# Kernel optimization log

Measured on AMD Instinct MI355X. Metric: run time of the kernel, lower is better.

The kernel has to match this reference:

```python
import jax, jax.numpy as jnp
import numpy as np

B, S, H, N, D = 2, 2048, 1024, 16, 64  # batch, seq, hidden, heads, head_dim


def setup_inputs() -> dict:
    key = jax.random.key(0)
    ks = jax.random.split(key, 7)
    sc = 0.02
    return {
        "query": jax.random.normal(ks[0], (B, S, H), jnp.float32),
        "key": jax.random.normal(ks[1], (B, S, H), jnp.float32),
        "value": jax.random.normal(ks[2], (B, S, H), jnp.float32),
        "Wq": jax.random.normal(ks[3], (N, H, D), jnp.float32) * sc,
        "Wk": jax.random.normal(ks[4], (N, H, D), jnp.float32) * sc,
        "Wv": jax.random.normal(ks[5], (N, H, D), jnp.float32) * sc,
        "Wo": jax.random.normal(ks[6], (H, H), jnp.float32) * sc,
    }


def reference(query, key, value, Wq, Wk, Wv, Wo):
    # Per-head projections (all heads batched): q,k,v -> [B, N, S, D]
    q = jnp.einsum('bsh,nhd->bnsd', query, Wq)
    k = jnp.einsum('bsh,nhd->bnsd', key, Wk)
    v = jnp.einsum('bsh,nhd->bnsd', value, Wv)
    scale = jnp.sqrt(jnp.asarray(D, q.dtype))
    # scaled dot-product attention, no mask, dropout=0 (eval mode)
    scores = jnp.einsum('bnqd,bnkd->bnqk', q, k) / scale  # [B, N, S, S]
    attn = jax.nn.softmax(scores, axis=-1)
    ctx = jnp.einsum('bnqk,bnkd->bnqd', attn, v)  # [B, N, S, D]
    # concat heads (head order matches the module's per-head list order)
    concat = ctx.transpose(0, 2, 1, 3).reshape(B, S, N * D)  # [B, S, H]
    out = concat @ Wo  # output projection, bias-free
    return out, attn
```

## Files before the change

kernel.cpp:

```cpp
#include <hip/hip_runtime.h>
#include <hip/hip_bf16.h>

using bf16 = __hip_bfloat16;
typedef __bf16 bf16x8 __attribute__((ext_vector_type(8)));
typedef __bf16 bf16x4 __attribute__((ext_vector_type(4)));
typedef float f32x4 __attribute__((ext_vector_type(4)));

__device__ __forceinline__ void async16(const void* g, void* l) {
    __builtin_amdgcn_global_load_lds((const __attribute__((address_space(1))) void*)g,
                                     (__attribute__((address_space(3))) void*)l, 16, 0, 0);
}
__device__ __forceinline__ bf16x8 ld8(const bf16* p) {
    return *reinterpret_cast<const bf16x8*>(p);
}
__device__ __forceinline__ unsigned short bfbits(float f) {
    bf16 h = __float2bfloat16(f);
    return *reinterpret_cast<unsigned short*>(&h);
}


__global__ __launch_bounds__(256) void cast_kernel(const float* __restrict__ q, const float* __restrict__ k,
                                                   const float* __restrict__ v, bf16* __restrict__ dst) {
    int z = blockIdx.z;
    const float* src = (z == 0) ? q : (z == 1) ? k : v;
    bf16* d = dst + (size_t)z * 4194304u;
    size_t i = ((size_t)blockIdx.x * 256 + threadIdx.x) * 4;
    float4 f = *(const float4*)(src + i);
    ushort4 pk = make_ushort4(bfbits(f.x), bfbits(f.y), bfbits(f.z), bfbits(f.w));
    *(ushort4*)(d + i) = pk;
}

__global__ __launch_bounds__(256) void wt_kernel(const float* __restrict__ wq, const float* __restrict__ wk,
                                                 const float* __restrict__ wv, bf16* __restrict__ wt) {
    int z = blockIdx.z;
    const float* W = (z == 0) ? wq : (z == 1) ? wk : wv;
    bf16* Wt = wt + (size_t)z * (1024u * 1024u);
    int n = blockIdx.y, h0 = blockIdx.x * 64;
    __shared__ float tile[64][65];
    int t = threadIdx.x, row = t >> 2, cq = t & 3;
#pragma unroll
    for (int u = 0; u < 4; u++) {
        int col = cq * 16 + u * 4;
        float4 f = *(const float4*)(W + (size_t)(n * 1024 + h0 + row) * 64 + col);
        tile[row][col] = f.x; tile[row][col + 1] = f.y; tile[row][col + 2] = f.z; tile[row][col + 3] = f.w;
    }
    __syncthreads();
#pragma unroll
    for (int u = 0; u < 4; u++) {
        int hl = cq * 16 + u * 4;
        ushort4 pk = make_ushort4(bfbits(tile[hl][row]), bfbits(tile[hl + 1][row]),
                                  bfbits(tile[hl + 2][row]), bfbits(tile[hl + 3][row]));
        *(ushort4*)(Wt + (size_t)(n * 64 + row) * 1024 + h0 + hl) = pk;
    }
}

__global__ __launch_bounds__(256) void wo_kernel(const float* __restrict__ Wo, bf16* __restrict__ Wot) {
    int h0 = blockIdx.x * 64, j0 = blockIdx.y * 64;
    __shared__ float tile[64][65];
    int t = threadIdx.x, row = t >> 2, cq = t & 3;
#pragma unroll
    for (int u = 0; u < 4; u++) {
        int col = cq * 16 + u * 4;
        float4 f = *(const float4*)(Wo + (size_t)(h0 + row) * 1024 + j0 + col);
        tile[row][col] = f.x; tile[row][col + 1] = f.y; tile[row][col + 2] = f.z; tile[row][col + 3] = f.w;
    }
    __syncthreads();
#pragma unroll
    for (int u = 0; u < 4; u++) {
        int hl = cq * 16 + u * 4;
        ushort4 pk = make_ushort4(bfbits(tile[hl][row]), bfbits(tile[hl + 1][row]),
                                  bfbits(tile[hl + 2][row]), bfbits(tile[hl + 3][row]));
        *(ushort4*)(Wot + (size_t)(j0 + row) * 1024 + h0 + hl) = pk;
    }
}

__global__ __launch_bounds__(256) void proj_kernel(const bf16* __restrict__ Xall, const bf16* __restrict__ Wall,
                                                   bf16* __restrict__ qb, bf16* __restrict__ kb,
                                                   bf16* __restrict__ vt) {
    int z = blockIdx.z;
    const bf16* X = Xall + (size_t)z * (4096u * 1024u);
    const bf16* W = Wall + (size_t)z * (1024u * 1024u);
    __shared__ bf16 sA[128 * 64];
    __shared__ bf16 sB[128 * 64];
    int t = threadIdx.x, lane = t & 63, q4 = lane >> 4, cl = lane & 15, w = t >> 6;
    int wm = (w >> 1) * 64, wn = (w & 1) * 64;
    int m0 = blockIdx.x * 128, n0 = blockIdx.y * 128;
    f32x4 acc[4][4] = {};
    for (int k0 = 0; k0 < 1024; k0 += 64) {
#pragma unroll
        for (int it = 0; it < 4; it++) {
            int j = it * 256 + t;
            int row = j >> 3, sl = j & 7, g = sl ^ (row & 7);
            async16(X + (size_t)(m0 + row) * 1024 + k0 + g * 8, sA + j * 8);
            async16(W + (size_t)(n0 + row) * 1024 + k0 + g * 8, sB + j * 8);
        }
        __syncthreads();
#pragma unroll
        for (int ks = 0; ks < 2; ks++) {
            bf16x8 af[4], bfr[4];
#pragma unroll
            for (int mi = 0; mi < 4; mi++) {
                int row = wm + mi * 16 + cl;
                af[mi] = ld8(sA + row * 64 + ((ks * 4 + q4) ^ (row & 7)) * 8);
            }
#pragma unroll
            for (int ni = 0; ni < 4; ni++) {
                int row = wn + ni * 16 + cl;
                bfr[ni] = ld8(sB + row * 64 + ((ks * 4 + q4) ^ (row & 7)) * 8);
            }
#pragma unroll
            for (int mi = 0; mi < 4; mi++)
#pragma unroll
                for (int ni = 0; ni < 4; ni++)
                    acc[mi][ni] = __builtin_amdgcn_mfma_f32_16x16x32_bf16(af[mi], bfr[ni], acc[mi][ni], 0, 0, 0);
        }
        __syncthreads();
    }
    if (z < 2) {
        bf16* dst = (z == 0) ? qb : kb;
        float qs = (z == 0) ? 0.18033688011112042f : 1.0f;
#pragma unroll
        for (int mi = 0; mi < 4; mi++)
#pragma unroll
            for (int ni = 0; ni < 4; ni++) {
                int col = n0 + wn + ni * 16 + cl;
                int hn = col >> 6, dd = col & 63;
#pragma unroll
                for (int i = 0; i < 4; i++) {
                    int row = m0 + wm + mi * 16 + q4 * 4 + i;
                    int b = row >> 11, s = row & 2047;
                    dst[(size_t)((b * 16 + hn) * 2048 + s) * 64 + dd] = __float2bfloat16(acc[mi][ni][i] * qs);
                }
            }
    } else {
#pragma unroll
        for (int mi = 0; mi < 4; mi++)
#pragma unroll
            for (int ni = 0; ni < 4; ni++) {
                int col = n0 + wn + ni * 16 + cl;
                int hn = col >> 6, dd = col & 63;
                int row0 = m0 + wm + mi * 16 + q4 * 4;
                int b = row0 >> 11, s = row0 & 2047;
                ushort4 pk = make_ushort4(bfbits(acc[mi][ni][0]), bfbits(acc[mi][ni][1]),
                                          bfbits(acc[mi][ni][2]), bfbits(acc[mi][ni][3]));
                *(ushort4*)(vt + (size_t)((b * 16 + hn) * 64 + dd) * 2048 + s) = pk;
            }
    }
}

__global__ __launch_bounds__(256) void attn_kernel(const bf16* __restrict__ qb, const bf16* __restrict__ kb,
                                                   const bf16* __restrict__ vt, bf16* __restrict__ cc,
                                                   float* __restrict__ attn) {
    __shared__ bf16 sQP[64 * 64];
    __shared__ bf16 sKb[64 * 64];
    __shared__ bf16 sVb[2][64 * 64];
    __shared__ float srow[64];
    __shared__ float sinv[64];
    int t = threadIdx.x, lane = t & 63, q4 = lane >> 4, cl = lane & 15, w = t >> 6;
    int bn = blockIdx.x;
    int s0 = blockIdx.y * 64;
    const bf16* qh = qb + (size_t)bn * 2048 * 64;
    const bf16* kh = kb + (size_t)bn * 2048 * 64;
    const bf16* vh = vt + (size_t)bn * 64 * 2048;
    float* ah = attn + (size_t)bn * 2048 * 2048;

    if (t < 64) srow[t] = 0.f;
#pragma unroll
    for (int it = 0; it < 2; it++) {
        int j = it * 256 + t;
        int row = j >> 3, sl = j & 7, g = sl ^ (row & 7);
        async16(qh + (size_t)(s0 + row) * 64 + g * 8, sQP + j * 8);
        async16(kh + (size_t)row * 64 + g * 8, sKb + j * 8);
    }
    __syncthreads();

    bf16x8 aq[4][2];
#pragma unroll
    for (int mi = 0; mi < 4; mi++)
#pragma unroll
        for (int ks = 0; ks < 2; ks++) {
            int row = mi * 16 + cl;
            aq[mi][ks] = ld8(sQP + row * 64 + ((ks * 4 + q4) ^ (row & 7)) * 8);
        }

    float rs[4][4] = {};
    for (int ch = 0; ch < 32; ch++) {
        const bf16* kcur = (ch & 1) ? sVb[0] : sKb;
        bf16* knxt = (ch & 1) ? sKb : sVb[0];
        if (ch < 31) {
#pragma unroll
            for (int it = 0; it < 2; it++) {
                int j = it * 256 + t;
                int row = j >> 3, sl = j & 7, g = sl ^ (row & 7);
                async16(kh + (size_t)((ch + 1) * 64 + row) * 64 + g * 8, knxt + j * 8);
            }
        }
        bf16x8 bk[2];
#pragma unroll
        for (int ks = 0; ks < 2; ks++) {
            int row = w * 16 + cl;
            bk[ks] = ld8(kcur + row * 64 + ((ks * 4 + q4) ^ (row & 7)) * 8);
        }
#pragma unroll
        for (int mi = 0; mi < 4; mi++) {
            f32x4 sa = {0.f, 0.f, 0.f, 0.f};
            sa = __builtin_amdgcn_mfma_f32_16x16x32_bf16(aq[mi][0], bk[0], sa, 0, 0, 0);
            sa = __builtin_amdgcn_mfma_f32_16x16x32_bf16(aq[mi][1], bk[1], sa, 0, 0, 0);
#pragma unroll
            for (int i = 0; i < 4; i++) rs[mi][i] += exp2f(sa[i]);
        }
        __syncthreads();
    }
#pragma unroll
    for (int mi = 0; mi < 4; mi++)
#pragma unroll
        for (int i = 0; i < 4; i++) {
            float v = rs[mi][i];
            v += __shfl_xor(v, 1);
            v += __shfl_xor(v, 2);
            v += __shfl_xor(v, 4);
            v += __shfl_xor(v, 8);
            if (cl == 0) atomicAdd(&srow[mi * 16 + q4 * 4 + i], v);
        }
    __syncthreads();
    if (t < 64) sinv[t] = 1.0f / srow[t];
    __syncthreads();
    float invC[4];
#pragma unroll
    for (int i = 0; i < 4; i++) invC[i] = sinv[w * 16 + q4 * 4 + i];

#pragma unroll
    for (int it = 0; it < 2; it++) {
        int j = it * 256 + t;
        int row = j >> 3, sl = j & 7, g = sl ^ (row & 7);
        async16(kh + (size_t)row * 64 + g * 8, sKb + j * 8);
        async16(vh + (size_t)row * 2048 + g * 8, sVb[0] + j * 8);
    }
    __syncthreads();

    f32x4 ctx[4] = {};
    for (int ch = 0; ch < 32; ch++) {
        int cur = ch & 1;
        if (ch < 31) {
#pragma unroll
            for (int it = 0; it < 2; it++) {
                int j = it * 256 + t;
                int row = j >> 3, sl = j & 7, g = sl ^ (row & 7);
                async16(vh + (size_t)row * 2048 + (ch + 1) * 64 + g * 8, sVb[cur ^ 1] + j * 8);
            }
        }
        __builtin_amdgcn_sched_barrier(0);
        bf16x8 bk[2];
#pragma unroll
        for (int ks = 0; ks < 2; ks++) {
            int row = w * 16 + cl;
            bk[ks] = ld8(sKb + row * 64 + ((ks * 4 + q4) ^ (row & 7)) * 8);
        }
        int c2 = w * 16 + cl;
#pragma unroll
        for (int mi = 0; mi < 4; mi++) {
            f32x4 sa = {0.f, 0.f, 0.f, 0.f};
            sa = __builtin_amdgcn_mfma_f32_16x16x32_bf16(aq[mi][0], bk[0], sa, 0, 0, 0);
            sa = __builtin_amdgcn_mfma_f32_16x16x32_bf16(aq[mi][1], bk[1], sa, 0, 0, 0);
#pragma unroll
            for (int i = 0; i < 4; i++) {
                float p = exp2f(sa[i]);
                int r = mi * 16 + q4 * 4 + i;
                sQP[r * 64 + ((c2 >> 3) ^ (r & 7)) * 8 + (c2 & 7)] = __float2bfloat16(p);
            }
        }
        asm volatile("s_waitcnt lgkmcnt(0)" ::: "memory");
        __builtin_amdgcn_sched_barrier(0);
        __builtin_amdgcn_s_barrier();
        if (ch < 31) {
#pragma unroll
            for (int it = 0; it < 2; it++) {
                int j = it * 256 + t;
                int row = j >> 3, sl = j & 7, g = sl ^ (row & 7);
                async16(kh + (size_t)((ch + 1) * 64 + row) * 64 + g * 8, sKb + j * 8);
            }
        }
        __builtin_amdgcn_sched_barrier(0);
        const bf16* vcur = sVb[cur];
#pragma unroll
        for (int ks = 0; ks < 2; ks++) {
            int rp = w * 16 + cl;
            bf16x8 ap = ld8(sQP + rp * 64 + ((ks * 4 + q4) ^ (rp & 7)) * 8);
#pragma unroll
            for (int ni = 0; ni < 4; ni++) {
                int rv = ni * 16 + cl;
                bf16x8 bv = ld8(vcur + rv * 64 + ((ks * 4 + q4) ^ (rv & 7)) * 8);
                ctx[ni] = __builtin_amdgcn_mfma_f32_16x16x32_bf16(ap, bv, ctx[ni], 0, 0, 0);
            }
        }
#pragma unroll
        for (int it = 0; it < 4; it++) {
            int j = it * 256 + t;
            int row = j >> 4, qc = j & 15;
            bf16x4 p4 = *reinterpret_cast<const bf16x4*>(sQP + row * 64 + ((qc >> 1) ^ (row & 7)) * 8 + (qc & 1) * 4);
            float inv = sinv[row];
            f32x4 o = {(float)p4[0] * inv, (float)p4[1] * inv, (float)p4[2] * inv, (float)p4[3] * inv};
            __builtin_nontemporal_store(o, reinterpret_cast<f32x4*>(ah + (size_t)(s0 + row) * 2048 + ch * 64 + qc * 4));
        }
        asm volatile("s_waitcnt vmcnt(4) lgkmcnt(0)" ::: "memory");
        __builtin_amdgcn_sched_barrier(0);
        __builtin_amdgcn_s_barrier();
    }
    int b = bn >> 4, n = bn & 15;
#pragma unroll
    for (int ni = 0; ni < 4; ni++)
#pragma unroll
        for (int i = 0; i < 4; i++) {
            int sg = s0 + w * 16 + q4 * 4 + i;
            int dd = ni * 16 + cl;
            cc[(size_t)(b * 2048 + sg) * 1024 + n * 64 + dd] = __float2bfloat16(ctx[ni][i] * invC[i]);
        }
}

__global__ __launch_bounds__(256) void out_kernel(const bf16* __restrict__ A, const bf16* __restrict__ W,
                                                  float* __restrict__ out) {
    __shared__ bf16 sA[128 * 64];
    __shared__ bf16 sB[128 * 64];
    int t = threadIdx.x, lane = t & 63, q4 = lane >> 4, cl = lane & 15, w = t >> 6;
    int wm = (w >> 1) * 64, wn = (w & 1) * 64;
    int m0 = blockIdx.x * 128, n0 = blockIdx.y * 128;
    f32x4 acc[4][4] = {};
    for (int k0 = 0; k0 < 1024; k0 += 64) {
#pragma unroll
        for (int it = 0; it < 4; it++) {
            int j = it * 256 + t;
            int row = j >> 3, sl = j & 7, g = sl ^ (row & 7);
            async16(A + (size_t)(m0 + row) * 1024 + k0 + g * 8, sA + j * 8);
            async16(W + (size_t)(n0 + row) * 1024 + k0 + g * 8, sB + j * 8);
        }
        __syncthreads();
#pragma unroll
        for (int ks = 0; ks < 2; ks++) {
            bf16x8 af[4], bfr[4];
#pragma unroll
            for (int mi = 0; mi < 4; mi++) {
                int row = wm + mi * 16 + cl;
                af[mi] = ld8(sA + row * 64 + ((ks * 4 + q4) ^ (row & 7)) * 8);
            }
#pragma unroll
            for (int ni = 0; ni < 4; ni++) {
                int row = wn + ni * 16 + cl;
                bfr[ni] = ld8(sB + row * 64 + ((ks * 4 + q4) ^ (row & 7)) * 8);
            }
#pragma unroll
            for (int mi = 0; mi < 4; mi++)
#pragma unroll
                for (int ni = 0; ni < 4; ni++)
                    acc[mi][ni] = __builtin_amdgcn_mfma_f32_16x16x32_bf16(af[mi], bfr[ni], acc[mi][ni], 0, 0, 0);
        }
        __syncthreads();
    }
#pragma unroll
    for (int mi = 0; mi < 4; mi++)
#pragma unroll
        for (int ni = 0; ni < 4; ni++) {
            int col = n0 + wn + ni * 16 + cl;
#pragma unroll
            for (int i = 0; i < 4; i++) {
                int row = m0 + wm + mi * 16 + q4 * 4 + i;
                out[(size_t)row * 1024 + col] = acc[mi][ni][i];
            }
        }
}

extern "C" void kernel_launch(void* const* d_in, const int* in_sizes, int n_in,
                              void* d_out, int out_size, void* d_ws, size_t ws_size,
                              hipStream_t stream) {
    const float* query = (const float*)d_in[0];
    const float* key = (const float*)d_in[1];
    const float* value = (const float*)d_in[2];
    const float* Wq = (const float*)d_in[3];
    const float* Wk = (const float*)d_in[4];
    const float* Wv = (const float*)d_in[5];
    const float* Wo = (const float*)d_in[6];
    float* out = (float*)d_out;
    float* attn = out + 4194304;

    char* w = (char*)d_ws;
    bf16* Xbf = (bf16*)(w);
    bf16* ccb = (bf16*)(w);
    bf16* Wt = (bf16*)(w + (24u << 20));
    bf16* Wot = (bf16*)(w + (30u << 20));
    bf16* qbuf = (bf16*)(w + (32u << 20));
    bf16* kbuf = (bf16*)(w + (40u << 20));
    bf16* vtb = (bf16*)(w + (48u << 20));

    cast_kernel<<<dim3(4096, 1, 3), 256, 0, stream>>>(query, key, value, Xbf);
    wt_kernel<<<dim3(16, 16, 3), 256, 0, stream>>>(Wq, Wk, Wv, Wt);
    wo_kernel<<<dim3(16, 16), 256, 0, stream>>>(Wo, Wot);
    proj_kernel<<<dim3(32, 8, 3), 256, 0, stream>>>(Xbf, Wt, qbuf, kbuf, vtb);
    attn_kernel<<<dim3(32, 32), 256, 0, stream>>>(qbuf, kbuf, vtb, ccb, attn);
    out_kernel<<<dim3(32, 8), 256, 0, stream>>>(ccb, Wot, out);
}
```

Measured before the change: 760.4 us.

## Repartition attention waves by query rows to drop cross-wave barriers

The attention kernel now gives each wave its own 16 query rows across all 64 key columns of a tile, instead of splitting the tile by key columns. Row sums therefore reduce inside a wave with shuffles, which removes the shared-memory atomic reduction and its extra barriers. It also removes the mid-iteration barrier between writing P and the PV product, since each wave only reads back its own P rows. K is now double-buffered and prefetched together with V, and s_setprio is raised around the MFMA sections. The cost is more LDS reads of K per wave, because every wave now loads all 64 K rows.

```diff
diff --git a/kernel.cpp b/kernel.cpp
--- a/kernel.cpp
+++ b/kernel.cpp
@@ -151,10 +151,9 @@
 __global__ __launch_bounds__(256) void attn_kernel(const bf16* __restrict__ qb, const bf16* __restrict__ kb,
                                                    const bf16* __restrict__ vt, bf16* __restrict__ cc,
                                                    float* __restrict__ attn) {
-    __shared__ bf16 sQP[64 * 64];
-    __shared__ bf16 sKb[64 * 64];
-    __shared__ bf16 sVb[2][64 * 64];
-    __shared__ float srow[64];
+    __shared__ bf16 sP[64 * 64];
+    __shared__ bf16 sK[2][64 * 64];
+    __shared__ bf16 sV[2][64 * 64];
     __shared__ float sinv[64];
     int t = threadIdx.x, lane = t & 63, q4 = lane >> 4, cl = lane & 15, w = t >> 6;
     int bn = blockIdx.x;
@@ -164,77 +163,67 @@
     const bf16* vh = vt + (size_t)bn * 64 * 2048;
     float* ah = attn + (size_t)bn * 2048 * 2048;
 
-    if (t < 64) srow[t] = 0.f;
 #pragma unroll
     for (int it = 0; it < 2; it++) {
         int j = it * 256 + t;
         int row = j >> 3, sl = j & 7, g = sl ^ (row & 7);
-        async16(qh + (size_t)(s0 + row) * 64 + g * 8, sQP + j * 8);
-        async16(kh + (size_t)row * 64 + g * 8, sKb + j * 8);
+        async16(qh + (size_t)(s0 + row) * 64 + g * 8, sP + j * 8);
+        async16(kh + (size_t)row * 64 + g * 8, sK[0] + j * 8);
     }
     __syncthreads();
 
-    bf16x8 aq[4][2];
-#pragma unroll
-    for (int mi = 0; mi < 4; mi++)
-#pragma unroll
-        for (int ks = 0; ks < 2; ks++) {
-            int row = mi * 16 + cl;
-            aq[mi][ks] = ld8(sQP + row * 64 + ((ks * 4 + q4) ^ (row & 7)) * 8);
-        }
-
-    float rs[4][4] = {};
+    bf16x8 aq[2];
+#pragma unroll
+    for (int ks = 0; ks < 2; ks++) {
+        int row = w * 16 + cl;
+        aq[ks] = ld8(sP + row * 64 + ((ks * 4 + q4) ^ (row & 7)) * 8);
+    }
+
+    float rs[4] = {0.f, 0.f, 0.f, 0.f};
     for (int ch = 0; ch < 32; ch++) {
-        const bf16* kcur = (ch & 1) ? sVb[0] : sKb;
-        bf16* knxt = (ch & 1) ? sKb : sVb[0];
+        int cur = ch & 1;
         if (ch < 31) {
 #pragma unroll
             for (int it = 0; it < 2; it++) {
                 int j = it * 256 + t;
                 int row = j >> 3, sl = j & 7, g = sl ^ (row & 7);
-                async16(kh + (size_t)((ch + 1) * 64 + row) * 64 + g * 8, knxt + j * 8);
-            }
-        }
-        bf16x8 bk[2];
-#pragma unroll
-        for (int ks = 0; ks < 2; ks++) {
-            int row = w * 16 + cl;
-            bk[ks] = ld8(kcur + row * 64 + ((ks * 4 + q4) ^ (row & 7)) * 8);
-        }
-#pragma unroll
-        for (int mi = 0; mi < 4; mi++) {
+                async16(kh + (size_t)((ch + 1) * 64 + row) * 64 + g * 8, sK[cur ^ 1] + j * 8);
+            }
+        }
+        __builtin_amdgcn_s_setprio(1);
+#pragma unroll
+        for (int ni = 0; ni < 4; ni++) {
             f32x4 sa = {0.f, 0.f, 0.f, 0.f};
-            sa = __builtin_amdgcn_mfma_f32_16x16x32_bf16(aq[mi][0], bk[0], sa, 0, 0, 0);
-            sa = __builtin_amdgcn_mfma_f32_16x16x32_bf16(aq[mi][1], bk[1], sa, 0, 0, 0);
-#pragma unroll
-            for (int i = 0; i < 4; i++) rs[mi][i] += exp2f(sa[i]);
-        }
-        __syncthreads();
-    }
-#pragma unroll
-    for (int mi = 0; mi < 4; mi++)
-#pragma unroll
-        for (int i = 0; i < 4; i++) {
-            float v = rs[mi][i];
-            v += __shfl_xor(v, 1);
-            v += __shfl_xor(v, 2);
-            v += __shfl_xor(v, 4);
-            v += __shfl_xor(v, 8);
-            if (cl == 0) atomicAdd(&srow[mi * 16 + q4 * 4 + i], v);
-        }
-    __syncthreads();
-    if (t < 64) sinv[t] = 1.0f / srow[t];
-    __syncthreads();
-    float invC[4];
-#pragma unroll
-    for (int i = 0; i < 4; i++) invC[i] = sinv[w * 16 + q4 * 4 + i];
+#pragma unroll
+            for (int ks = 0; ks < 2; ks++) {
+                int row = ni * 16 + cl;
+                bf16x8 bk = ld8(sK[cur] + row * 64 + ((ks * 4 + q4) ^ (row & 7)) * 8);
+                sa = __builtin_amdgcn_mfma_f32_16x16x32_bf16(aq[ks], bk, sa, 0, 0, 0);
+            }
+#pragma unroll
+            for (int i = 0; i < 4; i++) rs[i] += exp2f(sa[i]);
+        }
+        __builtin_amdgcn_s_setprio(0);
+        __syncthreads();
+    }
+    float invR[4];
+#pragma unroll
+    for (int i = 0; i < 4; i++) {
+        float v = rs[i];
+        v += __shfl_xor(v, 1);
+        v += __shfl_xor(v, 2);
+        v += __shfl_xor(v, 4);
+        v += __shfl_xor(v, 8);
+        invR[i] = 1.0f / v;
+        if (cl == 0) sinv[w * 16 + q4 * 4 + i] = invR[i];
+    }
 
 #pragma unroll
     for (int it = 0; it < 2; it++) {
         int j = it * 256 + t;
         int row = j >> 3, sl = j & 7, g = sl ^ (row & 7);
-        async16(kh + (size_t)row * 64 + g * 8, sKb + j * 8);
-        async16(vh + (size_t)row * 2048 + g * 8, sVb[0] + j * 8);
+        async16(kh + (size_t)row * 64 + g * 8, sK[0] + j * 8);
+        async16(vh + (size_t)row * 2048 + g * 8, sV[0] + j * 8);
     }
     __syncthreads();
 
@@ -246,65 +235,64 @@
             for (int it = 0; it < 2; it++) {
                 int j = it * 256 + t;
                 int row = j >> 3, sl = j & 7, g = sl ^ (row & 7);
-                async16(vh + (size_t)row * 2048 + (ch + 1) * 64 + g * 8, sVb[cur ^ 1] + j * 8);
+                async16(kh + (size_t)((ch + 1) * 64 + row) * 64 + g * 8, sK[cur ^ 1] + j * 8);
+                async16(vh + (size_t)row * 2048 + (ch + 1) * 64 + g * 8, sV[cur ^ 1] + j * 8);
             }
         }
         __builtin_amdgcn_sched_barrier(0);
-        bf16x8 bk[2];
+        f32x4 sa[4] = {};
+        __builtin_amdgcn_s_setprio(1);
 #pragma unroll
         for (int ks = 0; ks < 2; ks++) {
-            int row = w * 16 + cl;
-            bk[ks] = ld8(sKb + row * 64 + ((ks * 4 + q4) ^ (row & 7)) * 8);
-        }
-        int c2 = w * 16 + cl;
-#pragma unroll
-        for (int mi = 0; mi < 4; mi++) {
-            f32x4 sa = {0.f, 0.f, 0.f, 0.f};
-            sa = __builtin_amdgcn_mfma_f32_16x16x32_bf16(aq[mi][0], bk[0], sa, 0, 0, 0);
-            sa = __builtin_amdgcn_mfma_f32_16x16x32_bf16(aq[mi][1], bk[1], sa, 0, 0, 0);
+#pragma unroll
+            for (int ni = 0; ni < 4; ni++) {
+                int row = ni * 16 + cl;
+                bf16x8 bk = ld8(sK[cur] + row * 64 + ((ks * 4 + q4) ^ (row & 7)) * 8);
+                sa[ni] = __builtin_amdgcn_mfma_f32_16x16x32_bf16(aq[ks], bk, sa[ni], 0, 0, 0);
+            }
+        }
+        __builtin_amdgcn_s_setprio(0);
+        int r0 = w * 16 + q4 * 4;
+#pragma unroll
+        for (int ni = 0; ni < 4; ni++) {
+            int c2 = ni * 16 + cl;
 #pragma unroll
             for (int i = 0; i < 4; i++) {
-                float p = exp2f(sa[i]);
-                int r = mi * 16 + q4 * 4 + i;
-                sQP[r * 64 + ((c2 >> 3) ^ (r & 7)) * 8 + (c2 & 7)] = __float2bfloat16(p);
+                float p = exp2f(sa[ni][i]);
+                int r = r0 + i;
+                sP[r * 64 + ((c2 >> 3) ^ (r & 7)) * 8 + (c2 & 7)] = __float2bfloat16(p);
             }
         }
         asm volatile("s_waitcnt lgkmcnt(0)" ::: "memory");
         __builtin_amdgcn_sched_barrier(0);
-        __builtin_amdgcn_s_barrier();
-        if (ch < 31) {
-#pragma unroll
-            for (int it = 0; it < 2; it++) {
-                int j = it * 256 + t;
-                int row = j >> 3, sl = j & 7, g = sl ^ (row & 7);
-                async16(kh + (size_t)((ch + 1) * 64 + row) * 64 + g * 8, sKb + j * 8);
-            }
-        }
-        __builtin_amdgcn_sched_barrier(0);
-        const bf16* vcur = sVb[cur];
+        __builtin_amdgcn_s_setprio(1);
 #pragma unroll
         for (int ks = 0; ks < 2; ks++) {
             int rp = w * 16 + cl;
-            bf16x8 ap = ld8(sQP + rp * 64 + ((ks * 4 + q4) ^ (rp & 7)) * 8);
+            bf16x8 ap = ld8(sP + rp * 64 + ((ks * 4 + q4) ^ (rp & 7)) * 8);
 #pragma unroll
             for (int ni = 0; ni < 4; ni++) {
                 int rv = ni * 16 + cl;
-                bf16x8 bv = ld8(vcur + rv * 64 + ((ks * 4 + q4) ^ (rv & 7)) * 8);
+                bf16x8 bv = ld8(sV[cur] + rv * 64 + ((ks * 4 + q4) ^ (rv & 7)) * 8);
                 ctx[ni] = __builtin_amdgcn_mfma_f32_16x16x32_bf16(ap, bv, ctx[ni], 0, 0, 0);
             }
         }
+        __builtin_amdgcn_s_setprio(0);
 #pragma unroll
         for (int it = 0; it < 4; it++) {
-            int j = it * 256 + t;
-            int row = j >> 4, qc = j & 15;
-            bf16x4 p4 = *reinterpret_cast<const bf16x4*>(sQP + row * 64 + ((qc >> 1) ^ (row & 7)) * 8 + (qc & 1) * 4);
+            int idx = it * 64 + lane;
+            int rl = idx >> 4, qc = idx & 15;
+            int row = w * 16 + rl;
+            bf16x4 p4 = *reinterpret_cast<const bf16x4*>(sP + row * 64 + ((qc >> 1) ^ (row & 7)) * 8 + (qc & 1) * 4);
             float inv = sinv[row];
             f32x4 o = {(float)p4[0] * inv, (float)p4[1] * inv, (float)p4[2] * inv, (float)p4[3] * inv};
             __builtin_nontemporal_store(o, reinterpret_cast<f32x4*>(ah + (size_t)(s0 + row) * 2048 + ch * 64 + qc * 4));
         }
-        asm volatile("s_waitcnt vmcnt(4) lgkmcnt(0)" ::: "memory");
-        __builtin_amdgcn_sched_barrier(0);
-        __builtin_amdgcn_s_barrier();
+        if (ch < 31) {
+            asm volatile("s_waitcnt vmcnt(4) lgkmcnt(0)" ::: "memory");
+            __builtin_amdgcn_sched_barrier(0);
+            __builtin_amdgcn_s_barrier();
+        }
     }
     int b = bn >> 4, n = bn & 15;
 #pragma unroll
@@ -313,7 +301,7 @@
         for (int i = 0; i < 4; i++) {
             int sg = s0 + w * 16 + q4 * 4 + i;
             int dd = ni * 16 + cl;
-            cc[(size_t)(b * 2048 + sg) * 1024 + n * 64 + dd] = __float2bfloat16(ctx[ni][i] * invC[i]);
+            cc[(size_t)(b * 2048 + sg) * 1024 + n * 64 + dd] = __float2bfloat16(ctx[ni][i] * invR[i]);
         }
 }
 
```

New measurement: 755.4 us. Within noise of the previous version (-0.7%).
